# Optimization experiments

Measured on AMD Instinct MI355X. Metric: run time of the kernel, lower is better.

## Reference

```python
import jax, jax.numpy as jnp
import numpy as np

ROUTE_SCALE = 2.5
TOP_K = 2
N_EXPERTS = 16


def setup_inputs() -> dict:
    key = jax.random.key(0)
    ks = jax.random.split(key, 8)
    B, T, D, I, E = 2, 1024, 768, 384, N_EXPERTS
    s = 0.02
    return {
        "x": jax.random.normal(ks[0], (B, T, D), dtype=jnp.float32),
        "gate_w": jax.random.normal(ks[1], (E, D), dtype=jnp.float32) * s,
        "sg_w": jax.random.normal(ks[2], (I, D), dtype=jnp.float32) * s,
        "su_w": jax.random.normal(ks[3], (I, D), dtype=jnp.float32) * s,
        "sd_w": jax.random.normal(ks[4], (D, I), dtype=jnp.float32) * s,
        "rg_w": jax.random.normal(ks[5], (E, I, D), dtype=jnp.float32) * s,
        "ru_w": jax.random.normal(ks[6], (E, I, D), dtype=jnp.float32) * s,
        "rd_w": jax.random.normal(ks[7], (E, D, I), dtype=jnp.float32) * s,
    }


def _moe_forward(x, gate_w, sg_w, su_w, sd_w, rg_w, ru_w, rd_w):
    B, T, D = x.shape
    flat = x.reshape(-1, D)  # (N, D), N = B*T

    # ---- shared expert (SwiGLU FFN) ----
    g = flat @ sg_w.T
    u = flat @ su_w.T
    shared_out = (jax.nn.silu(g) * u) @ sd_w.T  # (N, D)

    # ---- gate: softmax(fp32) -> top-k -> renormalize ----
    logits = (flat @ gate_w.T) * ROUTE_SCALE  # (N, E)
    scores = jax.nn.softmax(logits.astype(jnp.float32), axis=-1)
    topk_w, topk_i = jax.lax.top_k(scores, TOP_K)  # (N, K)
    topk_w = topk_w / jnp.sum(topk_w, axis=-1, keepdims=True)
    topk_w = topk_w.astype(x.dtype)

    # aux load-balancing loss
    one_hot = jax.nn.one_hot(topk_i, N_EXPERTS, dtype=jnp.float32)  # (N, K, E)
    mask = one_hot.sum(axis=1)  # (N, E)
    f = mask.mean(axis=0)
    p = scores.mean(axis=0)
    aux_loss = jnp.sum(f * p) * N_EXPERTS

    # combine weights per (token, expert): sum_k w_k * [idx_k == e]
    combine = jnp.einsum("nk,nke->ne", topk_w, one_hot.astype(x.dtype))  # (N, E)

    # ---- routed experts as batched (grouped) SwiGLU GEMMs ----
    rg = jnp.einsum("nd,eid->nei", flat, rg_w)  # (N, E, I)
    ru = jnp.einsum("nd,eid->nei", flat, ru_w)
    rh = jax.nn.silu(rg) * ru  # (N, E, I)
    eo = jnp.einsum("nei,edi->ned", rh, rd_w)  # (N, E, D)
    routed_out = jnp.einsum("ned,ne->nd", eo, combine)  # (N, D)

    out = (shared_out + routed_out).reshape(B, T, D)
    return out, aux_loss


def reference(x, gate_w, sg_w, su_w, sd_w, rg_w, ru_w, rd_w):
    return _moe_forward(x, gate_w, sg_w, su_w, sd_w, rg_w, ru_w, rd_w)
```

## Files before the change

### kernel.cpp

```cpp
#include <hip/hip_runtime.h>
#include <math.h>

#define NTOK 2048
#define DDIM 768
#define IDIM 384
#define NEXP 16
#define XS_LD 776
#define HS_LD 392
#define NRT_MAX 144
#define NSHT 64
#define NWORK ((NSHT + NRT_MAX) * 6)
#define CHUNK (NWORK / 8)
#define ECAP 2048
#define HSHARED (NEXP * ECAP)
#define GBLK (NTOK / 4)

#define ZBLK 1536
#define CBLK (768 + 288 * 17 + 144 * 17)

typedef __attribute__((ext_vector_type(8))) short short8;
typedef __attribute__((ext_vector_type(4))) float f32x4;

__device__ __forceinline__ unsigned short f2bf(float f) {
    unsigned int u = __float_as_uint(f);
    unsigned int r = (u + 0x7fffu + ((u >> 16) & 1u)) >> 16;
    return (unsigned short)r;
}

#define WS_XB   1048576u
#define WS_W1F  4194304u
#define WS_WDF  24248320u
#define WS_H    34275328u

__global__ __launch_bounds__(256) void gate_kernel(
    const float* __restrict__ x, const float* __restrict__ gate_w,
    int* __restrict__ topk_i, float* __restrict__ topk_w,
    float* __restrict__ p_partial) {
    __shared__ float p_blk[16];
    int tid = threadIdx.x;
    if (tid < 16) p_blk[tid] = 0.f;
    __syncthreads();

    int wave = tid >> 6, lane = tid & 63;
    int n = blockIdx.x * 4 + wave;
    int e = lane >> 2, q = lane & 3;
    const float4* xr = (const float4*)(x + (size_t)n * DDIM);
    const float4* wr = (const float4*)(gate_w + (size_t)e * DDIM);
    float s = 0.f;
    #pragma unroll 4
    for (int k = q * 48; k < q * 48 + 48; ++k) {
        float4 a = xr[k], b = wr[k];
        s += a.x * b.x + a.y * b.y + a.z * b.z + a.w * b.w;
    }
    s += __shfl_xor(s, 1);
    s += __shfl_xor(s, 2);
    float logit = s * 2.5f;

    float m = logit;
    #pragma unroll
    for (int mask = 4; mask < 64; mask <<= 1)
        m = fmaxf(m, __shfl_xor(m, mask));
    float ex = __expf(logit - m);
    float sum = ex;
    #pragma unroll
    for (int mask = 4; mask < 64; mask <<= 1)
        sum += __shfl_xor(sum, mask);
    float sc = ex / sum;

    float v = sc; int idx = e;
    #pragma unroll
    for (int mask = 4; mask < 64; mask <<= 1) {
        float ov = __shfl_xor(v, mask);
        int   oi = __shfl_xor(idx, mask);
        if (ov > v || (ov == v && oi < idx)) { v = ov; idx = oi; }
    }
    float b0 = v; int i0 = idx;
    v = (e == i0) ? -1.f : sc; idx = e;
    #pragma unroll
    for (int mask = 4; mask < 64; mask <<= 1) {
        float ov = __shfl_xor(v, mask);
        int   oi = __shfl_xor(idx, mask);
        if (ov > v || (ov == v && oi < idx)) { v = ov; idx = oi; }
    }
    float b1 = v; int i1 = idx;
    float rs = 1.f / (b0 + b1);

    if (lane == 0) {
        topk_i[n * 2] = i0; topk_i[n * 2 + 1] = i1;
        topk_w[n * 2] = b0 * rs; topk_w[n * 2 + 1] = b1 * rs;
    }
    if (q == 0) atomicAdd(&p_blk[e], sc);
    __syncthreads();
    if (tid < 16) p_partial[blockIdx.x * 16 + tid] = p_blk[tid];
}

__global__ __launch_bounds__(256) void route_kernel(
    const int* __restrict__ topk_i, const float* __restrict__ topk_w,
    const float* __restrict__ p_partial,
    int* __restrict__ counts, int* __restrict__ perm_t, float* __restrict__ perm_w,
    float* __restrict__ out_aux) {
    __shared__ float s_p[256];
    __shared__ float s_psum[16];
    __shared__ int s_cnt[16];
    __shared__ int s_cur[16];
    int tid = threadIdx.x;
    {
        int e = tid & 15, g = tid >> 4;
        float acc = 0.f;
        for (int b = g; b < GBLK; b += 16) acc += p_partial[b * 16 + e];
        s_p[tid] = acc;
    }
    if (tid < 16) { s_cnt[tid] = 0; s_cur[tid] = 0; }
    __syncthreads();
    if (tid < 16) {
        float a = 0.f;
        #pragma unroll
        for (int g = 0; g < 16; ++g) a += s_p[g * 16 + tid];
        s_psum[tid] = a;
    }
    for (int n = tid; n < NTOK; n += 256) {
        atomicAdd(&s_cnt[topk_i[n * 2]], 1);
        atomicAdd(&s_cnt[topk_i[n * 2 + 1]], 1);
    }
    __syncthreads();
    if (tid < 16) counts[tid] = s_cnt[tid];
    if (tid == 0) {
        float a = 0.f;
        for (int e = 0; e < 16; ++e) a += (float)s_cnt[e] * s_psum[e];
        out_aux[0] = a * 16.f / ((float)NTOK * (float)NTOK);
    }
    for (int n = tid; n < NTOK; n += 256) {
        #pragma unroll
        for (int k = 0; k < 2; ++k) {
            int e = topk_i[n * 2 + k];
            int pos = atomicAdd(&s_cur[e], 1);
            perm_t[e * ECAP + pos] = n;
            perm_w[e * ECAP + pos] = topk_w[n * 2 + k];
        }
    }
}

__global__ __launch_bounds__(256) void convzero_kernel(
    const float* __restrict__ x,
    const float* __restrict__ rgw, const float* __restrict__ ruw,
    const float* __restrict__ sgw, const float* __restrict__ suw,
    const float* __restrict__ rdw, const float* __restrict__ sdw,
    float4* __restrict__ out4,
    unsigned short* __restrict__ xb, unsigned short* __restrict__ w1f,
    unsigned short* __restrict__ wdf) {
    int b = blockIdx.x, tid = threadIdx.x;

    if (b < ZBLK) {
        int i = b * 256 + tid;
        if (i < NTOK * DDIM / 4) out4[i] = make_float4(0.f, 0.f, 0.f, 0.f);
        return;
    }
    b -= ZBLK;

    const float* s;
    unsigned short* dst;
    if (b < 768) {
        int i = b * 256 + tid;
        s = x + (size_t)i * 8;
        dst = xb + (size_t)i * 8;
    } else if (b < 768 + 288 * 17) {
        int bb = b - 768;
        int E = bb / 288, bx = bb % 288;
        const float* gsrc = (E == 16) ? sgw : rgw + (size_t)E * (IDIM * DDIM);
        const float* usrc = (E == 16) ? suw : ruw + (size_t)E * (IDIM * DDIM);
        int i = bx * 256 + tid;
        int lane = i & 63;
        int fi = i >> 6;
        int ks = fi % 24, rg = fi / 24;
        int b16 = rg >> 1, gu = rg & 1;
        s = (gu ? usrc : gsrc)
          + (size_t)(b16 * 16 + (lane & 15)) * DDIM + ks * 32 + (lane >> 4) * 8;
        dst = w1f + (size_t)E * (DDIM * DDIM) + (size_t)i * 8;
    } else {
        int bb = b - (768 + 288 * 17);
        int E = bb / 144, bx = bb % 144;
        const float* src = (E == 16) ? sdw : rdw + (size_t)E * (DDIM * IDIM);
        int i = bx * 256 + tid;
        int lane = i & 63;
        int fi = i >> 6;
        int ks = fi % 12, cg = fi / 12;
        s = src + (size_t)(cg * 16 + (lane & 15)) * IDIM + ks * 32 + (lane >> 4) * 8;
        dst = wdf + (size_t)E * (DDIM * IDIM) + (size_t)i * 8;
    }
    float4 v0 = *(const float4*)s, v1 = *(const float4*)(s + 4);
    short8 o;
    o[0]=f2bf(v0.x); o[1]=f2bf(v0.y); o[2]=f2bf(v0.z); o[3]=f2bf(v0.w);
    o[4]=f2bf(v1.x); o[5]=f2bf(v1.y); o[6]=f2bf(v1.z); o[7]=f2bf(v1.w);
    *(short8*)dst = o;
}

__device__ __forceinline__ void swz_decode(int lid, int& bx, int& y) {
    int wid = (lid & 7) * CHUNK + (lid >> 3);
    bx = wid / 6;
    y = wid - bx * 6;
}

__device__ __forceinline__ bool tile_decode(const int* __restrict__ counts,
                                            int r, int& e, int& t, int& cnt) {
    int acc = 0;
    for (int ee = 0; ee < NEXP; ++ee) {
        int c = counts[ee];
        int tiles = (c + 31) >> 5;
        if (r < acc + tiles) { e = ee; t = r - acc; cnt = c; return true; }
        acc += tiles;
    }
    return false;
}

__global__ __launch_bounds__(256, 3) void p1_kernel(
    const unsigned short* __restrict__ xb, const unsigned short* __restrict__ w1f,
    const int* __restrict__ counts, const int* __restrict__ perm_t,
    unsigned short* __restrict__ h) {
    __shared__ unsigned short xs[32 * XS_LD];
    __shared__ int s_tok[32];

    int tid = threadIdx.x;
    int bx, y;
    swz_decode(blockIdx.x, bx, y);
    int e, hbase;
    if (bx < NSHT) {
        e = 16;
        hbase = HSHARED + bx * 32;
        if (tid < 32) s_tok[tid] = bx * 32 + tid;
    } else {
        int t, cnt;
        if (!tile_decode(counts, bx - NSHT, e, t, cnt)) return;
        hbase = e * ECAP + t * 32;
        if (tid < 32) {
            int slot = t * 32 + tid;
            s_tok[tid] = (slot < cnt) ? perm_t[e * ECAP + slot] : 0;
        }
    }
    __syncthreads();

    for (int c = tid; c < 32 * 96; c += 256) {
        int row = c / 96, off = (c - row * 96) * 8;
        *(short8*)(xs + row * XS_LD + off) =
            *(const short8*)(xb + (size_t)s_tok[row] * DDIM + off);
    }
    __syncthreads();

    int lane = tid & 63, wave = tid >> 6;
    int lr = lane & 15, kg = (lane >> 4) * 8, jrow = (lane >> 4) * 4;

    const unsigned short* pg = w1f + ((((size_t)e * 48 + (y * 8 + wave * 2    )) * 24) * 64 + lane) * 8;
    const unsigned short* pu = w1f + ((((size_t)e * 48 + (y * 8 + wave * 2 + 1)) * 24) * 64 + lane) * 8;

    f32x4 accg0 = (f32x4)0.f, accg1 = (f32x4)0.f, accu0 = (f32x4)0.f, accu1 = (f32x4)0.f;
    for (int ks = 0; ks < 24; ++ks) {
        short8 a0 = *(const short8*)(xs + lr * XS_LD + ks * 32 + kg);
        short8 a1 = *(const short8*)(xs + (16 + lr) * XS_LD + ks * 32 + kg);
        short8 bg = *(const short8*)(pg + (size_t)ks * 512);
        short8 bu = *(const short8*)(pu + (size_t)ks * 512);
        accg0 = __builtin_amdgcn_mfma_f32_16x16x32_bf16(a0, bg, accg0, 0, 0, 0);
        accg1 = __builtin_amdgcn_mfma_f32_16x16x32_bf16(a1, bg, accg1, 0, 0, 0);
        accu0 = __builtin_amdgcn_mfma_f32_16x16x32_bf16(a0, bu, accu0, 0, 0, 0);
        accu1 = __builtin_amdgcn_mfma_f32_16x16x32_bf16(a1, bu, accu1, 0, 0, 0);
    }

    int colg = y * 64 + wave * 16 + lr;
    #pragma unroll
    for (int m = 0; m < 2; ++m) {
        #pragma unroll
        for (int j = 0; j < 4; ++j) {
            int tl = m * 16 + jrow + j;
            float g = m ? accg1[j] : accg0[j];
            float u = m ? accu1[j] : accu0[j];
            float hv = g / (1.f + __expf(-g)) * u;
            h[(size_t)(hbase + tl) * IDIM + colg] = f2bf(hv);
        }
    }
}

__global__ __launch_bounds__(256, 4) void p2_kernel(
    const unsigned short* __restrict__ h, const unsigned short* __restrict__ wdf,
    const int* __restrict__ counts,
    const int* __restrict__ perm_t, const float* __restrict__ perm_w,
    float* __restrict__ out) {
    __shared__ unsigned short hs[32 * HS_LD];
    __shared__ int   s_tok[32];
    __shared__ float s_w[32];

    int tid = threadIdx.x;
    int bx, y;
    swz_decode(blockIdx.x, bx, y);
    int e, hbase;
    if (bx < NSHT) {
        e = 16;
        hbase = HSHARED + bx * 32;
        if (tid < 32) { s_tok[tid] = bx * 32 + tid; s_w[tid] = 1.f; }
    } else {
        int t, cnt;
        if (!tile_decode(counts, bx - NSHT, e, t, cnt)) return;
        hbase = e * ECAP + t * 32;
        if (tid < 32) {
            int slot = t * 32 + tid;
            bool v = slot < cnt;
            s_tok[tid] = v ? perm_t[e * ECAP + slot] : 0;
            s_w[tid]   = v ? perm_w[e * ECAP + slot] : 0.f;
        }
    }
    __syncthreads();

    for (int c = tid; c < 32 * 48; c += 256) {
        int row = c / 48, off = (c - row * 48) * 8;
        *(short8*)(hs + row * HS_LD + off) =
            *(const short8*)(h + (size_t)(hbase + row) * IDIM + off);
    }
    __syncthreads();

    int lane = tid & 63, wave = tid >> 6;
    int lr = lane & 15, kg = (lane >> 4) * 8, jrow = (lane >> 4) * 4;

    const unsigned short* p0 = wdf + ((((size_t)e * 48 + (y * 8 + wave * 2    )) * 12) * 64 + lane) * 8;
    const unsigned short* p1 = wdf + ((((size_t)e * 48 + (y * 8 + wave * 2 + 1)) * 12) * 64 + lane) * 8;

    f32x4 acc00 = (f32x4)0.f, acc01 = (f32x4)0.f, acc10 = (f32x4)0.f, acc11 = (f32x4)0.f;
    for (int ks = 0; ks < 12; ++ks) {
        short8 a0 = *(const short8*)(hs + lr * HS_LD + ks * 32 + kg);
        short8 a1 = *(const short8*)(hs + (16 + lr) * HS_LD + ks * 32 + kg);
        short8 b0 = *(const short8*)(p0 + (size_t)ks * 512);
        short8 b1 = *(const short8*)(p1 + (size_t)ks * 512);
        acc00 = __builtin_amdgcn_mfma_f32_16x16x32_bf16(a0, b0, acc00, 0, 0, 0);
        acc01 = __builtin_amdgcn_mfma_f32_16x16x32_bf16(a1, b0, acc01, 0, 0, 0);
        acc10 = __builtin_amdgcn_mfma_f32_16x16x32_bf16(a0, b1, acc10, 0, 0, 0);
        acc11 = __builtin_amdgcn_mfma_f32_16x16x32_bf16(a1, b1, acc11, 0, 0, 0);
    }

    int col0 = y * 128 + wave * 32 + lr;
    #pragma unroll
    for (int m = 0; m < 2; ++m) {
        #pragma unroll
        for (int j = 0; j < 4; ++j) {
            int tl = m * 16 + jrow + j;
            float w = s_w[tl];
            if (w == 0.f) continue;
            float* orow = out + (size_t)s_tok[tl] * DDIM;
            float v0 = m ? acc01[j] : acc00[j];
            float v1 = m ? acc11[j] : acc10[j];
            atomicAdd(orow + col0,      w * v0);
            atomicAdd(orow + col0 + 16, w * v1);
        }
    }
}

extern "C" void kernel_launch(void* const* d_in, const int* in_sizes, int n_in,
                              void* d_out, int out_size, void* d_ws, size_t ws_size,
                              hipStream_t stream) {
    const float* x      = (const float*)d_in[0];
    const float* gate_w = (const float*)d_in[1];
    const float* sg_w   = (const float*)d_in[2];
    const float* su_w   = (const float*)d_in[3];
    const float* sd_w   = (const float*)d_in[4];
    const float* rg_w   = (const float*)d_in[5];
    const float* ru_w   = (const float*)d_in[6];
    const float* rd_w   = (const float*)d_in[7];
    float* out = (float*)d_out;

    char* ws = (char*)d_ws;
    int*   counts    = (int*)(ws + 0);
    int*   perm_t    = (int*)(ws + 1024);
    float* perm_w    = (float*)(ws + 132096);
    float* p_partial = (float*)(ws + 263168);
    int*   topk_i    = (int*)(ws + 295936);
    float* topk_w    = (float*)(ws + 312320);
    unsigned short* xb  = (unsigned short*)(ws + WS_XB);
    unsigned short* w1f = (unsigned short*)(ws + WS_W1F);
    unsigned short* wdf = (unsigned short*)(ws + WS_WDF);
    unsigned short* hbuf= (unsigned short*)(ws + WS_H);

    gate_kernel<<<GBLK, 256, 0, stream>>>(x, gate_w, topk_i, topk_w, p_partial);

    convzero_kernel<<<ZBLK + CBLK, 256, 0, stream>>>(
        x, rg_w, ru_w, sg_w, su_w, rd_w, sd_w,
        (float4*)out, xb, w1f, wdf);

    route_kernel<<<1, 256, 0, stream>>>(topk_i, topk_w, p_partial,
                                        counts, perm_t, perm_w,
                                        out + (size_t)NTOK * DDIM);

    p1_kernel<<<NWORK, 256, 0, stream>>>(xb, w1f, counts, perm_t, hbuf);

    p2_kernel<<<NWORK, 256, 0, stream>>>(hbuf, wdf, counts, perm_t, perm_w, out);
}
```

Baseline: 105.0 us.

## Merge gate and convert kernels; widen GEMM token tiles to 64 rows

Fuses the gate computation into the zero/convert prep kernel, which removes one launch and lets the gate blocks overlap with the conversion blocks. Both expert GEMM phases now use 64-token tiles instead of 32, so each weight fragment loaded from global memory is reused across twice as many tokens. The first phase stages the token activations in two K halves to keep LDS usage bounded. The larger tiles leave fewer blocks, raise register pressure, and waste more padding on experts with few tokens.

After: 121.6 us. 1.16x slower.

```diff
diff --git a/kernel.cpp b/kernel.cpp
--- a/kernel.cpp
+++ b/kernel.cpp
@@ -5,18 +5,22 @@
 #define DDIM 768
 #define IDIM 384
 #define NEXP 16
-#define XS_LD 776
-#define HS_LD 392
-#define NRT_MAX 144
-#define NSHT 64
-#define NWORK ((NSHT + NRT_MAX) * 6)
-#define CHUNK (NWORK / 8)
 #define ECAP 2048
 #define HSHARED (NEXP * ECAP)
 #define GBLK (NTOK / 4)
 
+#define MT 64
+#define NSHT2 32
+#define NRT2 80
+#define NW2 ((NSHT2 + NRT2) * 6)
+#define CH2 (NW2 / 8)
+#define KH 384
+#define XS2_LD 392
+#define HS_LD 392
+
 #define ZBLK 1536
 #define CBLK (768 + 288 * 17 + 144 * 17)
+#define PREPBLK (ZBLK + CBLK + GBLK)
 
 typedef __attribute__((ext_vector_type(8))) short short8;
 typedef __attribute__((ext_vector_type(4))) float f32x4;
@@ -32,25 +36,79 @@
 #define WS_WDF  24248320u
 #define WS_H    34275328u
 
-__global__ __launch_bounds__(256) void gate_kernel(
+__global__ __launch_bounds__(256) void prep_kernel(
     const float* __restrict__ x, const float* __restrict__ gate_w,
+    const float* __restrict__ rgw, const float* __restrict__ ruw,
+    const float* __restrict__ sgw, const float* __restrict__ suw,
+    const float* __restrict__ rdw, const float* __restrict__ sdw,
+    float4* __restrict__ out4,
+    unsigned short* __restrict__ xb, unsigned short* __restrict__ w1f,
+    unsigned short* __restrict__ wdf,
     int* __restrict__ topk_i, float* __restrict__ topk_w,
     float* __restrict__ p_partial) {
     __shared__ float p_blk[16];
-    int tid = threadIdx.x;
+    int b = blockIdx.x, tid = threadIdx.x;
+
+    if (b < ZBLK) {
+        int i = b * 256 + tid;
+        if (i < NTOK * DDIM / 4) out4[i] = make_float4(0.f, 0.f, 0.f, 0.f);
+        return;
+    }
+    b -= ZBLK;
+
+    if (b < CBLK) {
+        const float* s;
+        unsigned short* dst;
+        if (b < 768) {
+            int i = b * 256 + tid;
+            s = x + (size_t)i * 8;
+            dst = xb + (size_t)i * 8;
+        } else if (b < 768 + 288 * 17) {
+            int bb = b - 768;
+            int E = bb / 288, bx = bb % 288;
+            const float* gsrc = (E == 16) ? sgw : rgw + (size_t)E * (IDIM * DDIM);
+            const float* usrc = (E == 16) ? suw : ruw + (size_t)E * (IDIM * DDIM);
+            int i = bx * 256 + tid;
+            int lane = i & 63;
+            int fi = i >> 6;
+            int ks = fi % 24, rg = fi / 24;
+            int b16 = rg >> 1, gu = rg & 1;
+            s = (gu ? usrc : gsrc)
+              + (size_t)(b16 * 16 + (lane & 15)) * DDIM + ks * 32 + (lane >> 4) * 8;
+            dst = w1f + (size_t)E * (DDIM * DDIM) + (size_t)i * 8;
+        } else {
+            int bb = b - (768 + 288 * 17);
+            int E = bb / 144, bx = bb % 144;
+            const float* src = (E == 16) ? sdw : rdw + (size_t)E * (DDIM * IDIM);
+            int i = bx * 256 + tid;
+            int lane = i & 63;
+            int fi = i >> 6;
+            int ks = fi % 12, cg = fi / 12;
+            s = src + (size_t)(cg * 16 + (lane & 15)) * IDIM + ks * 32 + (lane >> 4) * 8;
+            dst = wdf + (size_t)E * (DDIM * IDIM) + (size_t)i * 8;
+        }
+        float4 v0 = *(const float4*)s, v1 = *(const float4*)(s + 4);
+        short8 o;
+        o[0]=f2bf(v0.x); o[1]=f2bf(v0.y); o[2]=f2bf(v0.z); o[3]=f2bf(v0.w);
+        o[4]=f2bf(v1.x); o[5]=f2bf(v1.y); o[6]=f2bf(v1.z); o[7]=f2bf(v1.w);
+        *(short8*)dst = o;
+        return;
+    }
+    b -= CBLK;
+
     if (tid < 16) p_blk[tid] = 0.f;
     __syncthreads();
 
     int wave = tid >> 6, lane = tid & 63;
-    int n = blockIdx.x * 4 + wave;
+    int n = b * 4 + wave;
     int e = lane >> 2, q = lane & 3;
     const float4* xr = (const float4*)(x + (size_t)n * DDIM);
     const float4* wr = (const float4*)(gate_w + (size_t)e * DDIM);
     float s = 0.f;
     #pragma unroll 4
     for (int k = q * 48; k < q * 48 + 48; ++k) {
-        float4 a = xr[k], b = wr[k];
-        s += a.x * b.x + a.y * b.y + a.z * b.z + a.w * b.w;
+        float4 a = xr[k], bb = wr[k];
+        s += a.x * bb.x + a.y * bb.y + a.z * bb.z + a.w * bb.w;
     }
     s += __shfl_xor(s, 1);
     s += __shfl_xor(s, 2);
@@ -91,7 +149,7 @@
     }
     if (q == 0) atomicAdd(&p_blk[e], sc);
     __syncthreads();
-    if (tid < 16) p_partial[blockIdx.x * 16 + tid] = p_blk[tid];
+    if (tid < 16) p_partial[b * 16 + tid] = p_blk[tid];
 }
 
 __global__ __launch_bounds__(256) void route_kernel(
@@ -140,62 +198,8 @@
     }
 }
 
-__global__ __launch_bounds__(256) void convzero_kernel(
-    const float* __restrict__ x,
-    const float* __restrict__ rgw, const float* __restrict__ ruw,
-    const float* __restrict__ sgw, const float* __restrict__ suw,
-    const float* __restrict__ rdw, const float* __restrict__ sdw,
-    float4* __restrict__ out4,
-    unsigned short* __restrict__ xb, unsigned short* __restrict__ w1f,
-    unsigned short* __restrict__ wdf) {
-    int b = blockIdx.x, tid = threadIdx.x;
-
-    if (b < ZBLK) {
-        int i = b * 256 + tid;
-        if (i < NTOK * DDIM / 4) out4[i] = make_float4(0.f, 0.f, 0.f, 0.f);
-        return;
-    }
-    b -= ZBLK;
-
-    const float* s;
-    unsigned short* dst;
-    if (b < 768) {
-        int i = b * 256 + tid;
-        s = x + (size_t)i * 8;
-        dst = xb + (size_t)i * 8;
-    } else if (b < 768 + 288 * 17) {
-        int bb = b - 768;
-        int E = bb / 288, bx = bb % 288;
-        const float* gsrc = (E == 16) ? sgw : rgw + (size_t)E * (IDIM * DDIM);
-        const float* usrc = (E == 16) ? suw : ruw + (size_t)E * (IDIM * DDIM);
-        int i = bx * 256 + tid;
-        int lane = i & 63;
-        int fi = i >> 6;
-        int ks = fi % 24, rg = fi / 24;
-        int b16 = rg >> 1, gu = rg & 1;
-        s = (gu ? usrc : gsrc)
-          + (size_t)(b16 * 16 + (lane & 15)) * DDIM + ks * 32 + (lane >> 4) * 8;
-        dst = w1f + (size_t)E * (DDIM * DDIM) + (size_t)i * 8;
-    } else {
-        int bb = b - (768 + 288 * 17);
-        int E = bb / 144, bx = bb % 144;
-        const float* src = (E == 16) ? sdw : rdw + (size_t)E * (DDIM * IDIM);
-        int i = bx * 256 + tid;
-        int lane = i & 63;
-        int fi = i >> 6;
-        int ks = fi % 12, cg = fi / 12;
-        s = src + (size_t)(cg * 16 + (lane & 15)) * IDIM + ks * 32 + (lane >> 4) * 8;
-        dst = wdf + (size_t)E * (DDIM * IDIM) + (size_t)i * 8;
-    }
-    float4 v0 = *(const float4*)s, v1 = *(const float4*)(s + 4);
-    short8 o;
-    o[0]=f2bf(v0.x); o[1]=f2bf(v0.y); o[2]=f2bf(v0.z); o[3]=f2bf(v0.w);
-    o[4]=f2bf(v1.x); o[5]=f2bf(v1.y); o[6]=f2bf(v1.z); o[7]=f2bf(v1.w);
-    *(short8*)dst = o;
-}
-
 __device__ __forceinline__ void swz_decode(int lid, int& bx, int& y) {
-    int wid = (lid & 7) * CHUNK + (lid >> 3);
+    int wid = (lid & 7) * CH2 + (lid >> 3);
     bx = wid / 6;
     y = wid - bx * 6;
 }
@@ -205,7 +209,7 @@
     int acc = 0;
     for (int ee = 0; ee < NEXP; ++ee) {
         int c = counts[ee];
-        int tiles = (c + 31) >> 5;
+        int tiles = (c + 63) >> 6;
         if (r < acc + tiles) { e = ee; t = r - acc; cnt = c; return true; }
         acc += tiles;
     }
@@ -216,32 +220,25 @@
     const unsigned short* __restrict__ xb, const unsigned short* __restrict__ w1f,
     const int* __restrict__ counts, const int* __restrict__ perm_t,
     unsigned short* __restrict__ h) {
-    __shared__ unsigned short xs[32 * XS_LD];
-    __shared__ int s_tok[32];
+    __shared__ unsigned short xs[MT * XS2_LD];
+    __shared__ int s_tok[MT];
 
     int tid = threadIdx.x;
     int bx, y;
     swz_decode(blockIdx.x, bx, y);
     int e, hbase;
-    if (bx < NSHT) {
+    if (bx < NSHT2) {
         e = 16;
-        hbase = HSHARED + bx * 32;
-        if (tid < 32) s_tok[tid] = bx * 32 + tid;
+        hbase = HSHARED + bx * MT;
+        if (tid < MT) s_tok[tid] = bx * MT + tid;
     } else {
         int t, cnt;
-        if (!tile_decode(counts, bx - NSHT, e, t, cnt)) return;
-        hbase = e * ECAP + t * 32;
-        if (tid < 32) {
-            int slot = t * 32 + tid;
+        if (!tile_decode(counts, bx - NSHT2, e, t, cnt)) return;
+        hbase = e * ECAP + t * MT;
+        if (tid < MT) {
+            int slot = t * MT + tid;
             s_tok[tid] = (slot < cnt) ? perm_t[e * ECAP + slot] : 0;
         }
-    }
-    __syncthreads();
-
-    for (int c = tid; c < 32 * 96; c += 256) {
-        int row = c / 96, off = (c - row * 96) * 8;
-        *(short8*)(xs + row * XS_LD + off) =
-            *(const short8*)(xb + (size_t)s_tok[row] * DDIM + off);
     }
     __syncthreads();
 
@@ -251,55 +248,76 @@
     const unsigned short* pg = w1f + ((((size_t)e * 48 + (y * 8 + wave * 2    )) * 24) * 64 + lane) * 8;
     const unsigned short* pu = w1f + ((((size_t)e * 48 + (y * 8 + wave * 2 + 1)) * 24) * 64 + lane) * 8;
 
-    f32x4 accg0 = (f32x4)0.f, accg1 = (f32x4)0.f, accu0 = (f32x4)0.f, accu1 = (f32x4)0.f;
-    for (int ks = 0; ks < 24; ++ks) {
-        short8 a0 = *(const short8*)(xs + lr * XS_LD + ks * 32 + kg);
-        short8 a1 = *(const short8*)(xs + (16 + lr) * XS_LD + ks * 32 + kg);
-        short8 bg = *(const short8*)(pg + (size_t)ks * 512);
-        short8 bu = *(const short8*)(pu + (size_t)ks * 512);
-        accg0 = __builtin_amdgcn_mfma_f32_16x16x32_bf16(a0, bg, accg0, 0, 0, 0);
-        accg1 = __builtin_amdgcn_mfma_f32_16x16x32_bf16(a1, bg, accg1, 0, 0, 0);
-        accu0 = __builtin_amdgcn_mfma_f32_16x16x32_bf16(a0, bu, accu0, 0, 0, 0);
-        accu1 = __builtin_amdgcn_mfma_f32_16x16x32_bf16(a1, bu, accu1, 0, 0, 0);
+    f32x4 ag0 = (f32x4)0.f, ag1 = (f32x4)0.f, ag2 = (f32x4)0.f, ag3 = (f32x4)0.f;
+    f32x4 au0 = (f32x4)0.f, au1 = (f32x4)0.f, au2 = (f32x4)0.f, au3 = (f32x4)0.f;
+
+    #pragma unroll
+    for (int half = 0; half < 2; ++half) {
+        if (half) __syncthreads();
+        for (int c = tid; c < MT * 48; c += 256) {
+            int row = c / 48, off = (c - row * 48) * 8;
+            *(short8*)(xs + row * XS2_LD + off) =
+                *(const short8*)(xb + (size_t)s_tok[row] * DDIM + half * KH + off);
+        }
+        __syncthreads();
+
+        for (int ks = 0; ks < 12; ++ks) {
+            int ksg = half * 12 + ks;
+            short8 bg = *(const short8*)(pg + (size_t)ksg * 512);
+            short8 bu = *(const short8*)(pu + (size_t)ksg * 512);
+            short8 a0 = *(const short8*)(xs + (     lr) * XS2_LD + ks * 32 + kg);
+            short8 a1 = *(const short8*)(xs + (16 + lr) * XS2_LD + ks * 32 + kg);
+            short8 a2 = *(const short8*)(xs + (32 + lr) * XS2_LD + ks * 32 + kg);
+            short8 a3 = *(const short8*)(xs + (48 + lr) * XS2_LD + ks * 32 + kg);
+            ag0 = __builtin_amdgcn_mfma_f32_16x16x32_bf16(a0, bg, ag0, 0, 0, 0);
+            au0 = __builtin_amdgcn_mfma_f32_16x16x32_bf16(a0, bu, au0, 0, 0, 0);
+            ag1 = __builtin_amdgcn_mfma_f32_16x16x32_bf16(a1, bg, ag1, 0, 0, 0);
+            au1 = __builtin_amdgcn_mfma_f32_16x16x32_bf16(a1, bu, au1, 0, 0, 0);
+            ag2 = __builtin_amdgcn_mfma_f32_16x16x32_bf16(a2, bg, ag2, 0, 0, 0);
+            au2 = __builtin_amdgcn_mfma_f32_16x16x32_bf16(a2, bu, au2, 0, 0, 0);
+            ag3 = __builtin_amdgcn_mfma_f32_16x16x32_bf16(a3, bg, ag3, 0, 0, 0);
+            au3 = __builtin_amdgcn_mfma_f32_16x16x32_bf16(a3, bu, au3, 0, 0, 0);
+        }
     }
 
     int colg = y * 64 + wave * 16 + lr;
     #pragma unroll
-    for (int m = 0; m < 2; ++m) {
+    for (int mf = 0; mf < 4; ++mf) {
+        f32x4 g4 = (mf == 0) ? ag0 : (mf == 1) ? ag1 : (mf == 2) ? ag2 : ag3;
+        f32x4 u4 = (mf == 0) ? au0 : (mf == 1) ? au1 : (mf == 2) ? au2 : au3;
         #pragma unroll
         for (int j = 0; j < 4; ++j) {
-            int tl = m * 16 + jrow + j;
-            float g = m ? accg1[j] : accg0[j];
-            float u = m ? accu1[j] : accu0[j];
+            int tl = mf * 16 + jrow + j;
+            float g = g4[j], u = u4[j];
             float hv = g / (1.f + __expf(-g)) * u;
             h[(size_t)(hbase + tl) * IDIM + colg] = f2bf(hv);
         }
     }
 }
 
-__global__ __launch_bounds__(256, 4) void p2_kernel(
+__global__ __launch_bounds__(256, 3) void p2_kernel(
     const unsigned short* __restrict__ h, const unsigned short* __restrict__ wdf,
     const int* __restrict__ counts,
     const int* __restrict__ perm_t, const float* __restrict__ perm_w,
     float* __restrict__ out) {
-    __shared__ unsigned short hs[32 * HS_LD];
-    __shared__ int   s_tok[32];
-    __shared__ float s_w[32];
+    __shared__ unsigned short hs[MT * HS_LD];
+    __shared__ int   s_tok[MT];
+    __shared__ float s_w[MT];
 
     int tid = threadIdx.x;
     int bx, y;
     swz_decode(blockIdx.x, bx, y);
     int e, hbase;
-    if (bx < NSHT) {
+    if (bx < NSHT2) {
         e = 16;
-        hbase = HSHARED + bx * 32;
-        if (tid < 32) { s_tok[tid] = bx * 32 + tid; s_w[tid] = 1.f; }
+        hbase = HSHARED + bx * MT;
+        if (tid < MT) { s_tok[tid] = bx * MT + tid; s_w[tid] = 1.f; }
     } else {
         int t, cnt;
-        if (!tile_decode(counts, bx - NSHT, e, t, cnt)) return;
-        hbase = e * ECAP + t * 32;
-        if (tid < 32) {
-            int slot = t * 32 + tid;
+        if (!tile_decode(counts, bx - NSHT2, e, t, cnt)) return;
+        hbase = e * ECAP + t * MT;
+        if (tid < MT) {
+            int slot = t * MT + tid;
             bool v = slot < cnt;
             s_tok[tid] = v ? perm_t[e * ECAP + slot] : 0;
             s_w[tid]   = v ? perm_w[e * ECAP + slot] : 0.f;
@@ -307,7 +325,7 @@
     }
     __syncthreads();
 
-    for (int c = tid; c < 32 * 48; c += 256) {
+    for (int c = tid; c < MT * 48; c += 256) {
         int row = c / 48, off = (c - row * 48) * 8;
         *(short8*)(hs + row * HS_LD + off) =
             *(const short8*)(h + (size_t)(hbase + row) * IDIM + off);
@@ -320,31 +338,38 @@
     const unsigned short* p0 = wdf + ((((size_t)e * 48 + (y * 8 + wave * 2    )) * 12) * 64 + lane) * 8;
     const unsigned short* p1 = wdf + ((((size_t)e * 48 + (y * 8 + wave * 2 + 1)) * 12) * 64 + lane) * 8;
 
-    f32x4 acc00 = (f32x4)0.f, acc01 = (f32x4)0.f, acc10 = (f32x4)0.f, acc11 = (f32x4)0.f;
+    f32x4 c00 = (f32x4)0.f, c01 = (f32x4)0.f, c02 = (f32x4)0.f, c03 = (f32x4)0.f;
+    f32x4 c10 = (f32x4)0.f, c11 = (f32x4)0.f, c12 = (f32x4)0.f, c13 = (f32x4)0.f;
     for (int ks = 0; ks < 12; ++ks) {
-        short8 a0 = *(const short8*)(hs + lr * HS_LD + ks * 32 + kg);
-        short8 a1 = *(const short8*)(hs + (16 + lr) * HS_LD + ks * 32 + kg);
         short8 b0 = *(const short8*)(p0 + (size_t)ks * 512);
         short8 b1 = *(const short8*)(p1 + (size_t)ks * 512);
-        acc00 = __builtin_amdgcn_mfma_f32_16x16x32_bf16(a0, b0, acc00, 0, 0, 0);
-        acc01 = __builtin_amdgcn_mfma_f32_16x16x32_bf16(a1, b0, acc01, 0, 0, 0);
-        acc10 = __builtin_amdgcn_mfma_f32_16x16x32_bf16(a0, b1, acc10, 0, 0, 0);
-        acc11 = __builtin_amdgcn_mfma_f32_16x16x32_bf16(a1, b1, acc11, 0, 0, 0);
+        short8 a0 = *(const short8*)(hs + (     lr) * HS_LD + ks * 32 + kg);
+        short8 a1 = *(const short8*)(hs + (16 + lr) * HS_LD + ks * 32 + kg);
+        short8 a2 = *(const short8*)(hs + (32 + lr) * HS_LD + ks * 32 + kg);
+        short8 a3 = *(const short8*)(hs + (48 + lr) * HS_LD + ks * 32 + kg);
+        c00 = __builtin_amdgcn_mfma_f32_16x16x32_bf16(a0, b0, c00, 0, 0, 0);
+        c10 = __builtin_amdgcn_mfma_f32_16x16x32_bf16(a0, b1, c10, 0, 0, 0);
+        c01 = __builtin_amdgcn_mfma_f32_16x16x32_bf16(a1, b0, c01, 0, 0, 0);
+        c11 = __builtin_amdgcn_mfma_f32_16x16x32_bf16(a1, b1, c11, 0, 0, 0);
+        c02 = __builtin_amdgcn_mfma_f32_16x16x32_bf16(a2, b0, c02, 0, 0, 0);
+        c12 = __builtin_amdgcn_mfma_f32_16x16x32_bf16(a2, b1, c12, 0, 0, 0);
+        c03 = __builtin_amdgcn_mfma_f32_16x16x32_bf16(a3, b0, c03, 0, 0, 0);
+        c13 = __builtin_amdgcn_mfma_f32_16x16x32_bf16(a3, b1, c13, 0, 0, 0);
     }
 
     int col0 = y * 128 + wave * 32 + lr;
     #pragma unroll
-    for (int m = 0; m < 2; ++m) {
+    for (int mf = 0; mf < 4; ++mf) {
+        f32x4 v0 = (mf == 0) ? c00 : (mf == 1) ? c01 : (mf == 2) ? c02 : c03;
+        f32x4 v1 = (mf == 0) ? c10 : (mf == 1) ? c11 : (mf == 2) ? c12 : c13;
         #pragma unroll
         for (int j = 0; j < 4; ++j) {
-            int tl = m * 16 + jrow + j;
+            int tl = mf * 16 + jrow + j;
             float w = s_w[tl];
             if (w == 0.f) continue;
             float* orow = out + (size_t)s_tok[tl] * DDIM;
-            float v0 = m ? acc01[j] : acc00[j];
-            float v1 = m ? acc11[j] : acc10[j];
-            atomicAdd(orow + col0,      w * v0);
-            atomicAdd(orow + col0 + 16, w * v1);
+            atomicAdd(orow + col0,      w * v0[j]);
+            atomicAdd(orow + col0 + 16, w * v1[j]);
         }
     }
 }
@@ -374,17 +399,15 @@
     unsigned short* wdf = (unsigned short*)(ws + WS_WDF);
     unsigned short* hbuf= (unsigned short*)(ws + WS_H);
 
-    gate_kernel<<<GBLK, 256, 0, stream>>>(x, gate_w, topk_i, topk_w, p_partial);
-
-    convzero_kernel<<<ZBLK + CBLK, 256, 0, stream>>>(
-        x, rg_w, ru_w, sg_w, su_w, rd_w, sd_w,
-        (float4*)out, xb, w1f, wdf);
+    prep_kernel<<<PREPBLK, 256, 0, stream>>>(
+        x, gate_w, rg_w, ru_w, sg_w, su_w, rd_w, sd_w,
+        (float4*)out, xb, w1f, wdf, topk_i, topk_w, p_partial);
 
     route_kernel<<<1, 256, 0, stream>>>(topk_i, topk_w, p_partial,
                                         counts, perm_t, perm_w,
                                         out + (size_t)NTOK * DDIM);
 
-    p1_kernel<<<NWORK, 256, 0, stream>>>(xb, w1f, counts, perm_t, hbuf);
-
-    p2_kernel<<<NWORK, 256, 0, stream>>>(hbuf, wdf, counts, perm_t, perm_w, out);
-}
+    p1_kernel<<<NW2, 256, 0, stream>>>(xb, w1f, counts, perm_t, hbuf);
+
+    p2_kernel<<<NW2, 256, 0, stream>>>(hbuf, wdf, counts, perm_t, perm_w, out);
+}
```
